# Performance work log

Measured on AMD Instinct MI355X. Metric: run time of the kernel, lower is better.

The kernel has to match this reference:

```python
import jax, jax.numpy as jnp
import numpy as np

B, S, D, H = 2, 2048, 1024, 16
DK = D // H
SCALE = DK ** 0.5


def setup_inputs() -> dict:
    key = jax.random.key(0)
    ks = jax.random.split(key, 5)
    std = 1.0 / np.sqrt(D)
    return {
        "x": jax.random.normal(ks[0], (B, S, D), dtype=jnp.float32),
        "Wq": jax.random.normal(ks[1], (D, D), dtype=jnp.float32) * std,
        "Wk": jax.random.normal(ks[2], (D, D), dtype=jnp.float32) * std,
        "Wv": jax.random.normal(ks[3], (D, D), dtype=jnp.float32) * std,
        "Wo": jax.random.normal(ks[4], (D, D), dtype=jnp.float32) * std,
    }


def _split_heads(t):
    # [B, S, D] -> [B, H, S, DK]
    b, s, d = t.shape
    return t.reshape(b, s, H, DK).transpose(0, 2, 1, 3)


def reference(x, Wq, Wk, Wv, Wo):
    b, s, d = x.shape
    q = _split_heads(x @ Wq)
    k = _split_heads(x @ Wk)
    v = _split_heads(x @ Wv)
    # scores: [B, H, S, S]
    score = jnp.einsum("bhqd,bhkd->bhqk", q, k)
    causal = jnp.tril(jnp.ones((s, s), dtype=bool))[None, None]
    score = jnp.where(causal, score, -jnp.inf)
    attn = jax.nn.softmax(score / SCALE, axis=-1)
    out = jnp.einsum("bhqk,bhkd->bhqd", attn, v)
    out = out.transpose(0, 2, 1, 3).reshape(b, s, d)
    return out @ Wo
```

## Files before the change

kernel.cpp:

```cpp
#include <hip/hip_runtime.h>
#include <hip/hip_bf16.h>

typedef __bf16 bf16;
typedef __bf16 bf16x8 __attribute__((ext_vector_type(8)));
typedef float f32x4 __attribute__((ext_vector_type(4)));

#define MFMA16(a, b, c) __builtin_amdgcn_mfma_f32_16x16x32_bf16((a), (b), (c), 0, 0, 0)

__device__ __forceinline__ void async16(const void* g, void* l) {
  typedef const unsigned int __attribute__((address_space(1))) * GP;
  typedef unsigned int __attribute__((address_space(3))) * LP;
  __builtin_amdgcn_global_load_lds((GP)g, (LP)l, 16, 0, 0);
}

template <int ctrl>
__device__ __forceinline__ float dppf(float v) {
  return __builtin_bit_cast(
      float, __builtin_amdgcn_update_dpp(0, __builtin_bit_cast(int, v), ctrl,
                                         0xf, 0xf, true));
}
__device__ __forceinline__ float rowsum16(float x) {
  x += dppf<0xB1>(x);
  x += dppf<0x4E>(x);
  x += dppf<0x141>(x);
  x += dppf<0x140>(x);
  return x;
}

__global__ __launch_bounds__(256) void convert_x(
    const float* __restrict__ src, bf16* __restrict__ dst) {
  int i = (blockIdx.x * 256 + threadIdx.x) * 4;
  f32x4 v = *(const f32x4*)&src[i];
  bf16 o[4];
#pragma unroll
  for (int j = 0; j < 4; ++j) o[j] = (bf16)v[j];
  *(ulong1*)&dst[i] = *(ulong1*)o;
}

__global__ __launch_bounds__(256) void transpose_w(
    const float* __restrict__ w0, const float* __restrict__ w1,
    const float* __restrict__ w2, const float* __restrict__ w3,
    bf16* __restrict__ out) {
  __shared__ __align__(16) float tile[64][68];
  const float* src = (blockIdx.z == 0) ? w0 : (blockIdx.z == 1) ? w1
                   : (blockIdx.z == 2) ? w2 : w3;
  bf16* dst = out + (size_t)blockIdx.z * (1024u * 1024u);
  const int t = threadIdx.x;
  const int bx = blockIdx.x, by = blockIdx.y;

#pragma unroll
  for (int p = 0; p < 4; ++p) {
    int idx = t + p * 256;
    int r = idx >> 4, c4 = idx & 15;
    *(f32x4*)&tile[r][c4 * 4] =
        *(const f32x4*)&src[(size_t)(by * 64 + r) * 1024 + bx * 64 + c4 * 4];
  }
  __syncthreads();
#pragma unroll
  for (int p = 0; p < 2; ++p) {
    int idx = t + p * 256;
    int rn = idx >> 3, c8 = idx & 7;
    bf16x8 v;
#pragma unroll
    for (int i = 0; i < 8; ++i) v[i] = (bf16)tile[c8 * 8 + i][rn];
    *(bf16x8*)&dst[(size_t)(bx * 64 + rn) * 1024 + by * 64 + c8 * 8] = v;
  }
}

__global__ __launch_bounds__(256) void transpose_v(
    const bf16* __restrict__ v, bf16* __restrict__ vt) {
  __shared__ __align__(16) bf16 t[64][72];
  const int st = blockIdx.x, h = blockIdx.y, b = blockIdx.z;
  const int tid = threadIdx.x;
  const bf16* src = v + ((size_t)b * 2048) * 1024 + (size_t)h * 64;
  bf16* dst = vt + ((size_t)(b * 16 + h)) * 64 * 2048;
#pragma unroll
  for (int p = 0; p < 2; ++p) {
    int idx = tid + p * 256, r = idx >> 3, c = idx & 7;
    *(bf16x8*)&t[r][c * 8] =
        *(const bf16x8*)&src[(size_t)(st * 64 + r) * 1024 + c * 8];
  }
  __syncthreads();
#pragma unroll
  for (int p = 0; p < 2; ++p) {
    int idx = tid + p * 256, d = idx >> 3, c = idx & 7;
    bf16x8 o;
#pragma unroll
    for (int i = 0; i < 8; ++i) o[i] = t[c * 8 + i][d];
    *(bf16x8*)&dst[(size_t)d * 2048 + st * 64 + c * 8] = o;
  }
}

template <typename OutT>
__global__ __launch_bounds__(256, 4) void gemm_bt(
    const bf16* __restrict__ A, const bf16* __restrict__ Bt,
    OutT* __restrict__ C, int btStrideZ, int cStrideZ, float scaleZ0) {
  const int tid = threadIdx.x;
  const int wave = tid >> 6, lane = tid & 63;
  const int quad = lane >> 4, l16 = lane & 15;
  const int wm = wave >> 1, wn = wave & 1;
  const int m0 = blockIdx.y * 128, n0 = blockIdx.x * 128;
  const bf16* Bz = Bt + (size_t)blockIdx.z * (size_t)btStrideZ;
  OutT* Cz = C + (size_t)blockIdx.z * (size_t)cStrideZ;
  const float sc = (blockIdx.z == 0) ? scaleZ0 : 1.0f;

  __shared__ __align__(16) bf16 lsA[2][128 * 32];
  __shared__ __align__(16) bf16 lsB[2][128 * 32];

  const int lrow = lane >> 2;
  const int cgX = (lane & 3) ^ ((lrow >> 1) & 3);
  const int fR = (l16 >> 1) & 3;

  f32x4 acc[4][4];
#pragma unroll
  for (int i = 0; i < 4; ++i)
#pragma unroll
    for (int j = 0; j < 4; ++j) acc[i][j] = (f32x4){0.f, 0.f, 0.f, 0.f};

#pragma unroll
  for (int c = 0; c < 2; ++c) {
    int chunk = wave * 2 + c;
    int row = chunk * 16 + lrow;
    async16(&A[(size_t)(m0 + row) * 1024 + cgX * 8], &lsA[0][chunk * 512]);
    async16(&Bz[(size_t)(n0 + row) * 1024 + cgX * 8], &lsB[0][chunk * 512]);
  }
  __syncthreads();

  for (int it = 0; it < 32; ++it) {
    const int cur = it & 1;
    if (it < 31) {
      int k0n = (it + 1) * 32;
#pragma unroll
      for (int c = 0; c < 2; ++c) {
        int chunk = wave * 2 + c;
        int row = chunk * 16 + lrow;
        async16(&A[(size_t)(m0 + row) * 1024 + k0n + cgX * 8],
                &lsA[cur ^ 1][chunk * 512]);
        async16(&Bz[(size_t)(n0 + row) * 1024 + k0n + cgX * 8],
                &lsB[cur ^ 1][chunk * 512]);
      }
    }

    bf16x8 af[4], bfr[4];
#pragma unroll
    for (int i = 0; i < 4; ++i) {
      int ra = wm * 64 + i * 16 + l16;
      af[i] = *(const bf16x8*)&lsA[cur][ra * 32 + ((quad ^ fR) * 8)];
      int rb = wn * 64 + i * 16 + l16;
      bfr[i] = *(const bf16x8*)&lsB[cur][rb * 32 + ((quad ^ fR) * 8)];
    }
#pragma unroll
    for (int mi = 0; mi < 4; ++mi)
#pragma unroll
      for (int ni = 0; ni < 4; ++ni)
        acc[mi][ni] = MFMA16(af[mi], bfr[ni], acc[mi][ni]);

    __syncthreads();
  }

#pragma unroll
  for (int mi = 0; mi < 4; ++mi)
#pragma unroll
    for (int ni = 0; ni < 4; ++ni) {
      int col = n0 + wn * 64 + ni * 16 + l16;
#pragma unroll
      for (int r = 0; r < 4; ++r) {
        int row = m0 + wm * 64 + mi * 16 + quad * 4 + r;
        Cz[(size_t)row * 1024 + col] = (OutT)(acc[mi][ni][r] * sc);
      }
    }
}

__global__ __launch_bounds__(512, 4) void attn_fwd(
    const bf16* __restrict__ Q, const bf16* __restrict__ K,
    const bf16* __restrict__ Vt, bf16* __restrict__ O) {
  const int bid = blockIdx.x;
  const int x = bid & 15, hb = bid >> 4;
  const int h = hb & 15, b = hb >> 4;
  const int qt = b ? (15 - x) : x;
  const int tid = threadIdx.x;
  const int wave = tid >> 6, lane = tid & 63;
  const int quad = lane >> 4, l16 = lane & 15;

  __shared__ __align__(16) bf16 QsPs[128 * 64];
  __shared__ __align__(16) bf16 Ks[2][64 * 64];
  __shared__ __align__(16) bf16 Vs[2][64 * 64];

  const size_t base = ((size_t)b * 2048) * 1024 + (size_t)h * 64;
  const bf16* Qb = Q + base;
  const bf16* Kb = K + base;
  const bf16* Vtb = Vt + ((size_t)(b * 16 + h)) * 64 * 2048;
  bf16* Ob = O + base;

  const int lrow = lane >> 3;
  const int cgX = (lane & 7) ^ lrow;

#pragma unroll
  for (int c = 0; c < 2; ++c) {
    int chunk = wave * 2 + c;
    int row = chunk * 8 + lrow;
    async16(&Qb[(size_t)(qt * 128 + row) * 1024 + cgX * 8],
            &QsPs[chunk * 512]);
  }
  {
    int row = wave * 8 + lrow;
    async16(&Kb[(size_t)row * 1024 + cgX * 8], &Ks[0][wave * 512]);
    async16(&Vtb[(size_t)row * 2048 + cgX * 8], &Vs[0][wave * 512]);
  }
  __syncthreads();

  bf16x8 aq[2];
#pragma unroll
  for (int ks = 0; ks < 2; ++ks) {
    int row = wave * 16 + l16;
    aq[ks] =
        *(const bf16x8*)&QsPs[row * 64 + (((ks * 4 + quad) ^ (l16 & 7)) * 8)];
  }

  const float NEG_INF = -__builtin_inff();
  float ls_acc[4] = {0.f, 0.f, 0.f, 0.f};
  f32x4 Oacc[4];
#pragma unroll
  for (int nt = 0; nt < 4; ++nt) Oacc[nt] = (f32x4){0.f, 0.f, 0.f, 0.f};

  bf16* Psp = &QsPs[0];
  const int kt_end = 2 * qt + 1;
  const int ktd = 2 * qt + (wave >> 2);

  for (int kt = 0; kt <= kt_end; ++kt) {
    const int cur = kt & 1;
    if (kt < kt_end) {
      int row = wave * 8 + lrow;
      async16(&Kb[(size_t)((kt + 1) * 64 + row) * 1024 + cgX * 8],
              &Ks[cur ^ 1][wave * 512]);
      async16(&Vtb[(size_t)row * 2048 + (kt + 1) * 64 + cgX * 8],
              &Vs[cur ^ 1][wave * 512]);
    }

    if (kt <= ktd) {
      f32x4 sv[4];
#pragma unroll
      for (int nt = 0; nt < 4; ++nt) {
        int row = nt * 16 + l16;
        bf16x8 bk0 =
            *(const bf16x8*)&Ks[cur][row * 64 + ((quad ^ (l16 & 7)) * 8)];
        bf16x8 bk1 = *(const bf16x8*)&Ks[cur][row * 64 +
                                             (((4 + quad) ^ (l16 & 7)) * 8)];
        sv[nt] = (f32x4){0.f, 0.f, 0.f, 0.f};
        sv[nt] = MFMA16(aq[0], bk0, sv[nt]);
        sv[nt] = MFMA16(aq[1], bk1, sv[nt]);
      }

      if (kt == ktd) {
        const int rowb = wave * 16 + quad * 4;
        const int cb = (kt - 2 * qt) * 64;
#pragma unroll
        for (int nt = 0; nt < 4; ++nt) {
          const int col = cb + nt * 16 + l16;
#pragma unroll
          for (int r = 0; r < 4; ++r)
            if (col > rowb + r) sv[nt][r] = NEG_INF;
        }
      }
#pragma unroll
      for (int nt = 0; nt < 4; ++nt)
#pragma unroll
        for (int r = 0; r < 4; ++r) {
          float p = exp2f(sv[nt][r]);
          sv[nt][r] = p;
          ls_acc[r] += p;
        }

#pragma unroll
      for (int nt = 0; nt < 4; ++nt) {
        const int col = nt * 16 + l16;
        const int cg = col >> 3;
#pragma unroll
        for (int r = 0; r < 4; ++r) {
          int prow = wave * 16 + quad * 4 + r;
          Psp[prow * 64 + ((cg ^ (prow & 7)) * 8) + (col & 7)] =
              (bf16)sv[nt][r];
        }
      }

      const int arow = wave * 16 + l16;
      bf16x8 ap0 = *(const bf16x8*)&Psp[arow * 64 + ((quad ^ (l16 & 7)) * 8)];
      bf16x8 ap1 =
          *(const bf16x8*)&Psp[arow * 64 + (((4 + quad) ^ (l16 & 7)) * 8)];
#pragma unroll
      for (int nt = 0; nt < 4; ++nt) {
        int row = nt * 16 + l16;
        bf16x8 bv0 =
            *(const bf16x8*)&Vs[cur][row * 64 + ((quad ^ (l16 & 7)) * 8)];
        bf16x8 bv1 = *(const bf16x8*)&Vs[cur][row * 64 +
                                             (((4 + quad) ^ (l16 & 7)) * 8)];
        Oacc[nt] = MFMA16(ap0, bv0, Oacc[nt]);
        Oacc[nt] = MFMA16(ap1, bv1, Oacc[nt]);
      }
    }

    __syncthreads();
  }

  float rl[4];
#pragma unroll
  for (int r = 0; r < 4; ++r) rl[r] = 1.f / rowsum16(ls_acc[r]);
#pragma unroll
  for (int nt = 0; nt < 4; ++nt)
#pragma unroll
    for (int r = 0; r < 4; ++r) {
      int row = qt * 128 + wave * 16 + quad * 4 + r;
      Ob[(size_t)row * 1024 + nt * 16 + l16] = (bf16)(Oacc[nt][r] * rl[r]);
    }
}

extern "C" void kernel_launch(void* const* d_in, const int* in_sizes, int n_in,
                              void* d_out, int out_size, void* d_ws,
                              size_t ws_size, hipStream_t stream) {
  (void)in_sizes; (void)n_in; (void)out_size; (void)ws_size;
  const float* x  = (const float*)d_in[0];
  const float* Wq = (const float*)d_in[1];
  const float* Wk = (const float*)d_in[2];
  const float* Wv = (const float*)d_in[3];
  const float* Wo = (const float*)d_in[4];
  float* out = (float*)d_out;

  bf16* ws = (bf16*)d_ws;
  const size_t WELEM = 1024u * 1024u;
  const size_t TELEM = 4096u * 1024u;
  bf16* wt  = ws;
  bf16* xbf = ws + 4 * WELEM;
  bf16* q   = xbf + TELEM;
  bf16* k   = q + TELEM;
  bf16* v   = k + TELEM;
  bf16* ao  = v + TELEM;
  bf16* vt  = xbf;

  const float QSCALE = 0.125f * 1.44269504088896340736f;

  convert_x<<<dim3(4096), 256, 0, stream>>>(x, xbf);
  transpose_w<<<dim3(16, 16, 4), 256, 0, stream>>>(Wq, Wk, Wv, Wo, wt);
  gemm_bt<bf16><<<dim3(8, 32, 3), 256, 0, stream>>>(xbf, wt, q, (int)WELEM,
                                                    (int)TELEM, QSCALE);
  transpose_v<<<dim3(32, 16, 2), 256, 0, stream>>>(v, vt);
  attn_fwd<<<dim3(512), 512, 0, stream>>>(q, k, vt, ao);
  gemm_bt<float><<<dim3(8, 32, 1), 256, 0, stream>>>(ao, wt + 3 * WELEM, out,
                                                     0, 0, 1.0f);
}
```

Measured before the change: 195.5 us.

## Fuse V transpose into QKV GEMM epilogue and widen GEMM K-tile to 64

The QKV projection GEMM now writes the V output directly in transposed [B,H,DK,S] layout from its epilogue, which removes the separate transpose_v kernel and its extra read and write of V. The GEMM K-step also doubles from 32 to 64 with a new XOR swizzle, halving barrier iterations, and the LDS footprint doubles. To fit that, launch bounds drop from 4 to 2 blocks per SM. The transposed epilogue writes 8-byte strided stores, which may coalesce poorly, and the lower occupancy may reduce latency hiding.

```diff
diff --git a/kernel.cpp b/kernel.cpp
--- a/kernel.cpp
+++ b/kernel.cpp
@@ -67,34 +67,11 @@
   }
 }
 
-__global__ __launch_bounds__(256) void transpose_v(
-    const bf16* __restrict__ v, bf16* __restrict__ vt) {
-  __shared__ __align__(16) bf16 t[64][72];
-  const int st = blockIdx.x, h = blockIdx.y, b = blockIdx.z;
-  const int tid = threadIdx.x;
-  const bf16* src = v + ((size_t)b * 2048) * 1024 + (size_t)h * 64;
-  bf16* dst = vt + ((size_t)(b * 16 + h)) * 64 * 2048;
-#pragma unroll
-  for (int p = 0; p < 2; ++p) {
-    int idx = tid + p * 256, r = idx >> 3, c = idx & 7;
-    *(bf16x8*)&t[r][c * 8] =
-        *(const bf16x8*)&src[(size_t)(st * 64 + r) * 1024 + c * 8];
-  }
-  __syncthreads();
-#pragma unroll
-  for (int p = 0; p < 2; ++p) {
-    int idx = tid + p * 256, d = idx >> 3, c = idx & 7;
-    bf16x8 o;
-#pragma unroll
-    for (int i = 0; i < 8; ++i) o[i] = t[c * 8 + i][d];
-    *(bf16x8*)&dst[(size_t)d * 2048 + st * 64 + c * 8] = o;
-  }
-}
-
 template <typename OutT>
-__global__ __launch_bounds__(256, 4) void gemm_bt(
+__global__ __launch_bounds__(256, 2) void gemm_bt(
     const bf16* __restrict__ A, const bf16* __restrict__ Bt,
-    OutT* __restrict__ C, int btStrideZ, int cStrideZ, float scaleZ0) {
+    OutT* __restrict__ C, int btStrideZ, int cStrideZ, float scaleZ0,
+    bf16* __restrict__ vtOut) {
   const int tid = threadIdx.x;
   const int wave = tid >> 6, lane = tid & 63;
   const int quad = lane >> 4, l16 = lane & 15;
@@ -104,12 +81,11 @@
   OutT* Cz = C + (size_t)blockIdx.z * (size_t)cStrideZ;
   const float sc = (blockIdx.z == 0) ? scaleZ0 : 1.0f;
 
-  __shared__ __align__(16) bf16 lsA[2][128 * 32];
-  __shared__ __align__(16) bf16 lsB[2][128 * 32];
-
-  const int lrow = lane >> 2;
-  const int cgX = (lane & 3) ^ ((lrow >> 1) & 3);
-  const int fR = (l16 >> 1) & 3;
+  __shared__ __align__(16) bf16 lsA[2][128 * 64];
+  __shared__ __align__(16) bf16 lsB[2][128 * 64];
+
+  const int lrow = lane >> 3;
+  const int cgX = (lane & 7) ^ lrow;
 
   f32x4 acc[4][4];
 #pragma unroll
@@ -118,22 +94,22 @@
     for (int j = 0; j < 4; ++j) acc[i][j] = (f32x4){0.f, 0.f, 0.f, 0.f};
 
 #pragma unroll
-  for (int c = 0; c < 2; ++c) {
-    int chunk = wave * 2 + c;
-    int row = chunk * 16 + lrow;
+  for (int c = 0; c < 4; ++c) {
+    int chunk = wave * 4 + c;
+    int row = chunk * 8 + lrow;
     async16(&A[(size_t)(m0 + row) * 1024 + cgX * 8], &lsA[0][chunk * 512]);
     async16(&Bz[(size_t)(n0 + row) * 1024 + cgX * 8], &lsB[0][chunk * 512]);
   }
   __syncthreads();
 
-  for (int it = 0; it < 32; ++it) {
+  for (int it = 0; it < 16; ++it) {
     const int cur = it & 1;
-    if (it < 31) {
-      int k0n = (it + 1) * 32;
-#pragma unroll
-      for (int c = 0; c < 2; ++c) {
-        int chunk = wave * 2 + c;
-        int row = chunk * 16 + lrow;
+    if (it < 15) {
+      int k0n = (it + 1) * 64;
+#pragma unroll
+      for (int c = 0; c < 4; ++c) {
+        int chunk = wave * 4 + c;
+        int row = chunk * 8 + lrow;
         async16(&A[(size_t)(m0 + row) * 1024 + k0n + cgX * 8],
                 &lsA[cur ^ 1][chunk * 512]);
         async16(&Bz[(size_t)(n0 + row) * 1024 + k0n + cgX * 8],
@@ -141,34 +117,56 @@
       }
     }
 
-    bf16x8 af[4], bfr[4];
-#pragma unroll
-    for (int i = 0; i < 4; ++i) {
-      int ra = wm * 64 + i * 16 + l16;
-      af[i] = *(const bf16x8*)&lsA[cur][ra * 32 + ((quad ^ fR) * 8)];
-      int rb = wn * 64 + i * 16 + l16;
-      bfr[i] = *(const bf16x8*)&lsB[cur][rb * 32 + ((quad ^ fR) * 8)];
-    }
+#pragma unroll
+    for (int ks = 0; ks < 2; ++ks) {
+      bf16x8 af[4], bfr[4];
+#pragma unroll
+      for (int i = 0; i < 4; ++i) {
+        int ra = wm * 64 + i * 16 + l16;
+        af[i] = *(const bf16x8*)&lsA[cur][ra * 64 +
+                                          (((ks * 4 + quad) ^ (l16 & 7)) * 8)];
+        int rb = wn * 64 + i * 16 + l16;
+        bfr[i] = *(const bf16x8*)&lsB[cur][rb * 64 +
+                                           (((ks * 4 + quad) ^ (l16 & 7)) * 8)];
+      }
+#pragma unroll
+      for (int mi = 0; mi < 4; ++mi)
+#pragma unroll
+        for (int ni = 0; ni < 4; ++ni)
+          acc[mi][ni] = MFMA16(af[mi], bfr[ni], acc[mi][ni]);
+    }
+
+    __syncthreads();
+  }
+
+  if (blockIdx.z == 2 && vtOut != nullptr) {
 #pragma unroll
     for (int mi = 0; mi < 4; ++mi)
 #pragma unroll
-      for (int ni = 0; ni < 4; ++ni)
-        acc[mi][ni] = MFMA16(af[mi], bfr[ni], acc[mi][ni]);
-
-    __syncthreads();
-  }
-
-#pragma unroll
-  for (int mi = 0; mi < 4; ++mi)
-#pragma unroll
-    for (int ni = 0; ni < 4; ++ni) {
-      int col = n0 + wn * 64 + ni * 16 + l16;
-#pragma unroll
-      for (int r = 0; r < 4; ++r) {
-        int row = m0 + wm * 64 + mi * 16 + quad * 4 + r;
-        Cz[(size_t)row * 1024 + col] = (OutT)(acc[mi][ni][r] * sc);
-      }
-    }
+      for (int ni = 0; ni < 4; ++ni) {
+        int col = n0 + wn * 64 + ni * 16 + l16;
+        int h = col >> 6, d = col & 63;
+        int row = m0 + wm * 64 + mi * 16 + quad * 4;
+        int b = row >> 11, s = row & 2047;
+        bf16 o[4];
+#pragma unroll
+        for (int r = 0; r < 4; ++r) o[r] = (bf16)acc[mi][ni][r];
+        *(ulong1*)&vtOut[((size_t)(b * 16 + h) * 64 + d) * 2048 + s] =
+            *(ulong1*)o;
+      }
+  } else {
+#pragma unroll
+    for (int mi = 0; mi < 4; ++mi)
+#pragma unroll
+      for (int ni = 0; ni < 4; ++ni) {
+        int col = n0 + wn * 64 + ni * 16 + l16;
+#pragma unroll
+        for (int r = 0; r < 4; ++r) {
+          int row = m0 + wm * 64 + mi * 16 + quad * 4 + r;
+          Cz[(size_t)row * 1024 + col] = (OutT)(acc[mi][ni][r] * sc);
+        }
+      }
+  }
 }
 
 __global__ __launch_bounds__(512, 4) void attn_fwd(
@@ -332,18 +330,16 @@
   bf16* xbf = ws + 4 * WELEM;
   bf16* q   = xbf + TELEM;
   bf16* k   = q + TELEM;
-  bf16* v   = k + TELEM;
-  bf16* ao  = v + TELEM;
-  bf16* vt  = xbf;
+  bf16* vt  = k + TELEM;
+  bf16* ao  = vt + TELEM;
 
   const float QSCALE = 0.125f * 1.44269504088896340736f;
 
   convert_x<<<dim3(4096), 256, 0, stream>>>(x, xbf);
   transpose_w<<<dim3(16, 16, 4), 256, 0, stream>>>(Wq, Wk, Wv, Wo, wt);
   gemm_bt<bf16><<<dim3(8, 32, 3), 256, 0, stream>>>(xbf, wt, q, (int)WELEM,
-                                                    (int)TELEM, QSCALE);
-  transpose_v<<<dim3(32, 16, 2), 256, 0, stream>>>(v, vt);
+                                                    (int)TELEM, QSCALE, vt);
   attn_fwd<<<dim3(512), 512, 0, stream>>>(q, k, vt, ao);
   gemm_bt<float><<<dim3(8, 32, 1), 256, 0, stream>>>(ao, wt + 3 * WELEM, out,
-                                                     0, 0, 1.0f);
-}
+                                                     0, 0, 1.0f, nullptr);
+}
```

Result: slower. 209.9 us (+7.4%).
